# Performance work log

Measured on AMD Instinct MI355X. Metric: run time of the kernel, lower is better.

Reference implementation:

```python
import jax, jax.numpy as jnp
import numpy as np

EPS = 1e-5  # torch LayerNorm default

def _std(x):
    # standardize over the last 3 (tensor-feature) modes, biased variance like torch LayerNorm
    mu = jnp.mean(x, axis=(-3, -2, -1), keepdims=True)
    var = jnp.mean(jnp.square(x - mu), axis=(-3, -2, -1), keepdims=True)
    return (x - mu) * jax.lax.rsqrt(var + EPS)

def setup_inputs() -> dict:
    key = jax.random.key(0)
    ks = jax.random.split(key, 12)
    T, B = 512, 16
    a = b = c = 16          # input tensor modes (4096 features)
    ha = hb = hc = 8        # hidden tensor modes (512 features)
    G = 3                   # gates: r, z, n
    f32 = jnp.float32
    return {
        "x": jax.random.normal(ks[0], (T, B, a, b, c), f32),
        "h0": jnp.zeros((B, ha, hb, hc), f32),
        # input-to-hidden TCL3D factors + rank-1 bias + LN affines (stacked over 3 gates)
        "W_fa": jax.random.normal(ks[1], (G, a, ha), f32),
        "W_fb": jax.random.normal(ks[2], (G, b, hb), f32),
        "W_fc": jax.random.normal(ks[3], (G, c, hc), f32),
        "W_ba": jax.random.normal(ks[4], (G, ha), f32),
        "W_bb": jax.random.normal(ks[5], (G, hb), f32),
        "W_bc": jax.random.normal(ks[6], (G, hc), f32),
        "W_lnin_w": jnp.ones((G, a, b, c), f32),
        "W_lnin_b": jnp.zeros((G, a, b, c), f32),
        "W_lnout_w": jnp.ones((G, ha, hb, hc), f32),
        "W_lnout_b": jnp.zeros((G, ha, hb, hc), f32),
        # hidden-to-hidden TCL3D factors + rank-1 bias + LN affines
        "U_fa": jax.random.normal(ks[7], (G, ha, ha), f32),
        "U_fb": jax.random.normal(ks[8], (G, hb, hb), f32),
        "U_fc": jax.random.normal(ks[9], (G, hc, hc), f32),
        "U_ba": jax.random.normal(ks[10], (G, ha), f32),
        "U_bb": jax.random.normal(ks[11], (G, hb), f32),
        "U_bc": jax.random.normal(jax.random.fold_in(key, 99), (G, hc), f32),
        "U_lnin_w": jnp.ones((G, ha, hb, hc), f32),
        "U_lnin_b": jnp.zeros((G, ha, hb, hc), f32),
        "U_lnout_w": jnp.ones((G, ha, hb, hc), f32),
        "U_lnout_b": jnp.zeros((G, ha, hb, hc), f32),
    }

def reference(x, h0, W_fa, W_fb, W_fc, W_ba, W_bb, W_bc,
              W_lnin_w, W_lnin_b, W_lnout_w, W_lnout_b,
              U_fa, U_fb, U_fc, U_ba, U_bb, U_bc,
              U_lnin_w, U_lnin_b, U_lnout_w, U_lnout_b):
    # --- input-to-hidden TCL3D for all 3 gates, batched over time (no h dependence) ---
    xh = _std(x)                                                  # [T,B,a,b,c]
    xg = xh[None] * W_lnin_w[:, None, None] + W_lnin_b[:, None, None]  # [3,T,B,a,b,c]
    Wx = jnp.einsum('gtnabc,gad,gbe,gcf->gtndef', xg, W_fa, W_fb, W_fc)
    Wx = Wx + (W_ba[:, None, None, :, None, None]
               * W_bb[:, None, None, None, :, None]
               * W_bc[:, None, None, None, None, :])              # rank-1 bias
    Wx = _std(Wx) * W_lnout_w[:, None, None] + W_lnout_b[:, None, None]
    Wx = jnp.swapaxes(Wx, 0, 1)                                   # [T,3,B,ha,hb,hc]

    Ub = (U_ba[:, None, :, None, None]
          * U_bb[:, None, None, :, None]
          * U_bc[:, None, None, None, :])                         # [3,1,ha,hb,hc]

    def step(h, wx):
        # hidden-to-hidden TCL3D for all 3 gates
        hh = _std(h)                                              # [B,ha,hb,hc]
        hg = hh[None] * U_lnin_w[:, None] + U_lnin_b[:, None]     # [3,B,ha,hb,hc]
        Uh = jnp.einsum('gndef,gdp,geq,gfr->gnpqr', hg, U_fa, U_fb, U_fc) + Ub
        Uh = _std(Uh) * U_lnout_w[:, None] + U_lnout_b[:, None]
        r = jax.nn.sigmoid(wx[0] + Uh[0])
        z = jax.nn.sigmoid(wx[1] + Uh[1])
        n = jnp.tanh(wx[2] + r * Uh[2])
        h_new = (1.0 - z) * n + z * h
        return h_new, h_new

    _, outs = jax.lax.scan(step, h0, Wx)                          # [T,B,ha,hb,hc]
    return outs
```

## Files before the change

### kernel.cpp

```cpp
#include <hip/hip_runtime.h>

#define EPSV 1e-5f

#define KEEPV(x) asm volatile("" : "+v"(x))
#define KEEPS(x) asm volatile("" : "+s"(x))

#define DPP_XADD(v, ctrl)                                                  \
    v += __int_as_float(__builtin_amdgcn_update_dpp(                       \
        0, __float_as_int(v), ctrl, 0xF, 0xF, false))

__device__ __forceinline__ float wave_allsum(float v) {
    DPP_XADD(v, 0x128);
    DPP_XADD(v, 0x124);
    DPP_XADD(v, 0x122);
    DPP_XADD(v, 0x121);
    DPP_XADD(v, 0x142);
    DPP_XADD(v, 0x143);
    return __int_as_float(__builtin_amdgcn_readlane(__float_as_int(v), 63));
}

__device__ __forceinline__ void bar_lds() {
    asm volatile("s_waitcnt lgkmcnt(0)\n\ts_barrier" ::: "memory");
}

__global__ __launch_bounds__(256) void wx_kernel(
    const float* __restrict__ x,
    const float* __restrict__ Wfa, const float* __restrict__ Wfb,
    const float* __restrict__ Wfc,
    const float* __restrict__ Wba, const float* __restrict__ Wbb,
    const float* __restrict__ Wbc,
    const float* __restrict__ lniw, const float* __restrict__ lnib,
    const float* __restrict__ lnow, const float* __restrict__ lnob,
    float* __restrict__ wxo)
{
    __shared__ float Xs[4096];
    __shared__ float S1[2048];
    __shared__ float S2[1024];
    __shared__ float baS[24], bbS[24], bcS[24];
    __shared__ float red[16];

    const int tid  = threadIdx.x;
    const int wid  = tid >> 6, lane = tid & 63;
    const size_t tb = blockIdx.x;
    const float* xp = x + tb * 4096;

    float s = 0.f, s2 = 0.f;
    for (int i = tid; i < 4096; i += 256) {
        float v = xp[i];
        Xs[i] = v;
        s += v; s2 += v * v;
    }
    if (tid < 24) { baS[tid] = Wba[tid]; bbS[tid] = Wbb[tid]; bcS[tid] = Wbc[tid]; }

    __syncthreads();
    #pragma unroll
    for (int off = 32; off > 0; off >>= 1) {
        s  += __shfl_down(s,  off);
        s2 += __shfl_down(s2, off);
    }
    if (lane == 0) { red[wid] = s; red[8 + wid] = s2; }
    __syncthreads();
    s  = red[0] + red[1] + red[2] + red[3];
    s2 = red[8] + red[9] + red[10] + red[11];
    const float muX = s * (1.f / 4096.f);
    const float rsX = rsqrtf(fmaxf(s2 * (1.f / 4096.f) - muX * muX, 0.f) + EPSV);

    const int qh = __builtin_amdgcn_readfirstlane(tid >> 7);
    const int rh = __builtin_amdgcn_readfirstlane(tid >> 6);

    for (int g = 0; g < 3; ++g) {
        {
            float acc[8] = {0,0,0,0,0,0,0,0};
            const int rest = tid;
            const float* lw = lniw + g * 4096;
            const float* lb = lnib + g * 4096;
            #pragma unroll
            for (int m = 0; m < 16; ++m) {
                const float xn = (Xs[m*256 + rest] - muX) * rsX;
                const float xv = fmaf(xn, lw[m*256 + rest], lb[m*256 + rest]);
                #pragma unroll
                for (int p = 0; p < 8; ++p)
                    acc[p] = fmaf(xv, Wfa[(g*16 + m)*8 + p], acc[p]);
            }
            #pragma unroll
            for (int p = 0; p < 8; ++p)
                S1[p*256 + (rest ^ (p << 3))] = acc[p];
        }
        __syncthreads();
        {
            float acc[4] = {0,0,0,0};
            const int rest2 = tid & 127;
            const int c2 = rest2 >> 3, p2 = rest2 & 7;
            #pragma unroll
            for (int m = 0; m < 16; ++m) {
                const float xv = S1[p2*256 + (((m << 4) | c2) ^ (p2 << 3))];
                #pragma unroll
                for (int j = 0; j < 4; ++j)
                    acc[j] = fmaf(xv, Wfb[(g*16 + m)*8 + qh*4 + j], acc[j]);
            }
            #pragma unroll
            for (int j = 0; j < 4; ++j) {
                const int q = qh*4 + j;
                S2[q*128 + (rest2 ^ (q << 3))] = acc[j];
            }
        }
        __syncthreads();
        float v0, v1; int idx0;
        {
            float acc[2] = {0, 0};
            const int rest3 = tid & 63;
            const int q3 = rest3 & 7, pp = rest3 >> 3;
            #pragma unroll
            for (int m = 0; m < 16; ++m) {
                const float xv = S2[q3*128 + (((m << 3) | pp) ^ (q3 << 3))];
                #pragma unroll
                for (int j = 0; j < 2; ++j)
                    acc[j] = fmaf(xv, Wfc[(g*16 + m)*8 + rh*2 + j], acc[j]);
            }
            const float bpq = baS[g*8 + pp] * bbS[g*8 + q3];
            v0 = acc[0] + bpq * bcS[g*8 + rh*2 + 0];
            v1 = acc[1] + bpq * bcS[g*8 + rh*2 + 1];
            idx0 = rest3 * 8 + rh * 2;
        }
        float t = v0 + v1, t2 = v0*v0 + v1*v1;
        __syncthreads();
        #pragma unroll
        for (int off = 32; off > 0; off >>= 1) {
            t  += __shfl_down(t,  off);
            t2 += __shfl_down(t2, off);
        }
        if (lane == 0) { red[wid] = t; red[8 + wid] = t2; }
        __syncthreads();
        t  = red[0] + red[1] + red[2] + red[3];
        t2 = red[8] + red[9] + red[10] + red[11];
        const float mu  = t * (1.f / 512.f);
        const float var = fmaxf(t2 * (1.f / 512.f) - mu * mu, 0.f);
        const float rs  = rsqrtf(var + EPSV);
        float* wp = wxo + (tb * 3 + g) * 512;
        const float2 lw2 = *(const float2*)(lnow + g*512 + idx0);
        const float2 lb2 = *(const float2*)(lnob + g*512 + idx0);
        float2 o2;
        o2.x = fmaf((v0 - mu) * rs, lw2.x, lb2.x);
        o2.y = fmaf((v1 - mu) * rs, lw2.y, lb2.y);
        *(float2*)(wp + idx0) = o2;
    }
}

__global__ __launch_bounds__(192)
__attribute__((amdgpu_waves_per_eu(1, 1)))
void scan_kernel(
    const float* __restrict__ wx,
    const float* __restrict__ h0,
    const float* __restrict__ Ufa, const float* __restrict__ Ufb,
    const float* __restrict__ Ufc,
    const float* __restrict__ Uba, const float* __restrict__ Ubb,
    const float* __restrict__ Ubc,
    const float* __restrict__ lniw, const float* __restrict__ lnib,
    const float* __restrict__ lnow, const float* __restrict__ lnob,
    float* __restrict__ out,
    int T, int B)
{
    const int n    = blockIdx.x;
    const int tid  = threadIdx.x;
    const int lane = tid & 63;
    const int gu   = __builtin_amdgcn_readfirstlane(tid >> 6);

    __shared__ float hgS[3][576];
    __shared__ float T1S[3][576];
    __shared__ float T2S[3][576];
    __shared__ float UhS[2][3][576];

    float wA[64], wB[64], wC[64];
    #pragma unroll
    for (int i = 0; i < 64; ++i) {
        wA[i] = __uint_as_float(__builtin_amdgcn_readfirstlane(
                    __float_as_uint(Ufa[gu*64 + i])));
        KEEPS(wA[i]);
    }
    #pragma unroll
    for (int i = 0; i < 64; ++i) { wB[i] = Ufb[gu*64 + i]; KEEPV(wB[i]); }
    #pragma unroll
    for (int i = 0; i < 64; ++i) { wC[i] = Ufc[gu*64 + i]; KEEPV(wC[i]); }

    float lnwT[8], lnbT[8], low8[8], lob8[8], ubias[8];
    {
        const int p_ = lane >> 3, q_ = lane & 7;
        const float bpq = Uba[gu*8 + p_] * Ubb[gu*8 + q_];
        #pragma unroll
        for (int k = 0; k < 8; ++k) {
            lnwT[k]  = lniw[gu*512 + k*64 + lane];
            lnbT[k]  = lnib[gu*512 + k*64 + lane];
            low8[k]  = lnow[gu*512 + lane*8 + k];
            lob8[k]  = lnob[gu*512 + lane*8 + k];
            ubias[k] = bpq * Ubc[gu*8 + k];
        }
    }

    const int wbase = lane;
    const int rbase = (lane & 7) * 72 + (lane >> 3);

    float hv[8];
    {
        const float4 a = *(const float4*)(h0 + n*512 + lane*8);
        const float4 b = *(const float4*)(h0 + n*512 + lane*8 + 4);
        hv[0]=a.x; hv[1]=a.y; hv[2]=a.z; hv[3]=a.w;
        hv[4]=b.x; hv[5]=b.y; hv[6]=b.z; hv[7]=b.w;
    }

    float uo[8];
    float pf[3][8];

#define LOADWX(TT)                                                         \
    {                                                                      \
        const float* base_ = wx + (((size_t)(TT) * B + n) * 3) * 512       \
                             + lane * 8;                                   \
        _Pragma("unroll")                                                  \
        for (int gg = 0; gg < 3; ++gg) {                                   \
            const float4 A_ = *(const float4*)(base_ + gg*512);            \
            const float4 B_ = *(const float4*)(base_ + gg*512 + 4);        \
            pf[gg][0]=A_.x; pf[gg][1]=A_.y; pf[gg][2]=A_.z; pf[gg][3]=A_.w;\
            pf[gg][4]=B_.x; pf[gg][5]=B_.y; pf[gg][6]=B_.z; pf[gg][7]=B_.w;\
        }                                                                  \
    }

#define WR8(BUFROW, V)                                                     \
    {                                                                      \
        float* p0_ = (BUFROW) + wbase;                                     \
        float* p1_ = p0_ + 288;                                            \
        p0_[0] = V[0]; p0_[72] = V[1]; p0_[144] = V[2]; p0_[216] = V[3];   \
        p1_[0] = V[4]; p1_[72] = V[5]; p1_[144] = V[6]; p1_[216] = V[7];   \
    }

#define RD8(BUFROW, V)                                                     \
    {                                                                      \
        const float* q_ = (BUFROW) + rbase;                                \
        V[0] = q_[0];  V[1] = q_[8];  V[2] = q_[16]; V[3] = q_[24];        \
        V[4] = q_[32]; V[5] = q_[40]; V[6] = q_[48]; V[7] = q_[56];        \
    }

#define RD8W(BUFROW, V)                                                    \
    {                                                                      \
        const float* q0_ = (BUFROW) + wbase;                               \
        const float* q1_ = q0_ + 288;                                      \
        V[0] = q0_[0]; V[1] = q0_[72]; V[2] = q0_[144]; V[3] = q0_[216];   \
        V[4] = q1_[0]; V[5] = q1_[72]; V[6] = q1_[144]; V[7] = q1_[216];   \
    }

#define PIPELINE(PARN)                                                     \
    {                                                                      \
         \
         \
        float xv_[8];                                                      \
        RD8(hgS[gu], xv_)                                                  \
        float sA = 0.f, sB = 0.f;                                          \
        _Pragma("unroll")                                                  \
        for (int k = 0; k < 8; ++k) { sA += hv[k]; sB += hv[k]*hv[k]; }    \
        sA = wave_allsum(sA); sB = wave_allsum(sB);                        \
        const float mu_ = sA * (1.f/512.f);                                \
        const float rs_ = rsqrtf(fmaxf(sB*(1.f/512.f) - mu_*mu_, 0.f)      \
                                 + EPSV);                                  \
        float a_[8];                                                       \
        _Pragma("unroll") for (int k = 0; k < 8; ++k) a_[k] = 0.f;         \
        _Pragma("unroll")                                                  \
        for (int m = 0; m < 8; ++m) {                                      \
            const float hgv = fmaf((xv_[m]-mu_)*rs_, lnwT[m], lnbT[m]);    \
            _Pragma("unroll")                                              \
            for (int q = 0; q < 8; ++q)                                    \
                a_[q] = fmaf(hgv, wA[m*8 + q], a_[q]);                     \
        }                                                                  \
        WR8(T1S[gu], a_)                                                   \
        RD8(T1S[gu], xv_)                                                  \
        _Pragma("unroll") for (int k = 0; k < 8; ++k) a_[k] = 0.f;         \
        _Pragma("unroll")                                                  \
        for (int m = 0; m < 8; ++m) {                                      \
            _Pragma("unroll")                                              \
            for (int q = 0; q < 8; ++q)                                    \
                a_[q] = fmaf(xv_[m], wB[m*8 + q], a_[q]);                  \
        }                                                                  \
        WR8(T2S[gu], a_)                                                   \
        RD8(T2S[gu], xv_)                                                  \
        _Pragma("unroll") for (int k = 0; k < 8; ++k) a_[k] = 0.f;         \
        _Pragma("unroll")                                                  \
        for (int m = 0; m < 8; ++m) {                                      \
            _Pragma("unroll")                                              \
            for (int q = 0; q < 8; ++q)                                    \
                a_[q] = fmaf(xv_[m], wC[m*8 + q], a_[q]);                  \
        }                                                                  \
        float sC = 0.f, sD = 0.f;                                          \
        _Pragma("unroll")                                                  \
        for (int k = 0; k < 8; ++k) {                                      \
            a_[k] += ubias[k]; sC += a_[k]; sD += a_[k]*a_[k];             \
        }                                                                  \
        sC = wave_allsum(sC); sD = wave_allsum(sD);                        \
        const float mu2_ = sC * (1.f/512.f);                               \
        const float rs2_ = rsqrtf(fmaxf(sD*(1.f/512.f) - mu2_*mu2_, 0.f)   \
                                  + EPSV);                                 \
        _Pragma("unroll")                                                  \
        for (int k = 0; k < 8; ++k)                                        \
            uo[k] = fmaf((a_[k]-mu2_)*rs2_, low8[k], lob8[k]);             \
        WR8(UhS[PARN][gu], uo)                                             \
    }

#define COMBINE(PARC, TT)                                                  \
    {                                                                      \
        float ur[8], uz[8], un[8];                                         \
        if (gu == 0) {                                                     \
            _Pragma("unroll")                                              \
            for (int k = 0; k < 8; ++k) ur[k] = uo[k];                     \
            RD8W(UhS[PARC][1], uz)                                         \
            RD8W(UhS[PARC][2], un)                                         \
        } else if (gu == 1) {                                              \
            _Pragma("unroll")                                              \
            for (int k = 0; k < 8; ++k) uz[k] = uo[k];                     \
            RD8W(UhS[PARC][0], ur)                                         \
            RD8W(UhS[PARC][2], un)                                         \
        } else {                                                           \
            _Pragma("unroll")                                              \
            for (int k = 0; k < 8; ++k) un[k] = uo[k];                     \
            RD8W(UhS[PARC][0], ur)                                         \
            RD8W(UhS[PARC][1], uz)                                         \
        }                                                                  \
        _Pragma("unroll")                                                  \
        for (int k = 0; k < 8; ++k) {                                      \
            const float er_ = __expf(-(pf[0][k] + ur[k]));                 \
            const float r_  = __builtin_amdgcn_rcpf(1.f + er_);            \
            const float ez_ = __expf(-(pf[1][k] + uz[k]));                 \
            const float z_  = __builtin_amdgcn_rcpf(1.f + ez_);            \
            const float e2_ = __expf(2.f * (pf[2][k] + r_ * un[k]));       \
            const float nn_ = 1.f - 2.f*__builtin_amdgcn_rcpf(e2_ + 1.f);  \
            hv[k] = (1.f - z_)*nn_ + z_*hv[k];                             \
        }                                                                  \
        WR8(hgS[gu], hv)      \
        if (gu == 0) {                                                     \
            float* op_ = out + ((size_t)(TT) * B + n) * 512 + lane*8;      \
            *(float4*)op_     = make_float4(hv[0], hv[1], hv[2], hv[3]);   \
            *(float4*)(op_+4) = make_float4(hv[4], hv[5], hv[6], hv[7]);   \
        }                                                                  \
    }

    LOADWX(0);
    WR8(hgS[gu], hv)
    PIPELINE(0);

    for (int t = 0; t < T; t += 2) {
        bar_lds();
        COMBINE(0, t)
        if (t + 1 < T) {
            LOADWX(t + 1);
            PIPELINE(1)
        }
        bar_lds();
        if (t + 1 < T) COMBINE(1, t + 1)
        if (t + 2 < T) {
            LOADWX(t + 2);
            PIPELINE(0)
        }
    }
#undef LOADWX
#undef WR8
#undef RD8
#undef RD8W
#undef PIPELINE
#undef COMBINE
}

extern "C" void kernel_launch(void* const* d_in, const int* in_sizes, int n_in,
                              void* d_out, int out_size, void* d_ws, size_t ws_size,
                              hipStream_t stream)
{
    const float* x    = (const float*)d_in[0];
    const float* h0   = (const float*)d_in[1];
    const float* Wfa  = (const float*)d_in[2];
    const float* Wfb  = (const float*)d_in[3];
    const float* Wfc  = (const float*)d_in[4];
    const float* Wba  = (const float*)d_in[5];
    const float* Wbb  = (const float*)d_in[6];
    const float* Wbc  = (const float*)d_in[7];
    const float* Wliw = (const float*)d_in[8];
    const float* Wlib = (const float*)d_in[9];
    const float* Wlow = (const float*)d_in[10];
    const float* Wlob = (const float*)d_in[11];
    const float* Ufa  = (const float*)d_in[12];
    const float* Ufb  = (const float*)d_in[13];
    const float* Ufc  = (const float*)d_in[14];
    const float* Uba  = (const float*)d_in[15];
    const float* Ubb  = (const float*)d_in[16];
    const float* Ubc  = (const float*)d_in[17];
    const float* Uliw = (const float*)d_in[18];
    const float* Ulib = (const float*)d_in[19];
    const float* Ulow = (const float*)d_in[20];
    const float* Ulob = (const float*)d_in[21];

    const int B = in_sizes[1] / 512;
    const int T = in_sizes[0] / (B * 4096);

    float* wxws = (float*)d_ws;
    float* out  = (float*)d_out;

    wx_kernel<<<T * B, 256, 0, stream>>>(x, Wfa, Wfb, Wfc, Wba, Wbb, Wbc,
                                         Wliw, Wlib, Wlow, Wlob, wxws);
    scan_kernel<<<B, 192, 0, stream>>>(wxws, h0, Ufa, Ufb, Ufc, Uba, Ubb, Ubc,
                                       Uliw, Ulib, Ulow, Ulob, out, T, B);
}
```

Measured before the change: 805.7 us.

## Process all three gates together in wx_kernel and vectorize input loads

The input-projection kernel now computes all three gates in a single pass through each TCL stage instead of looping over gates. This cuts the block-wide barriers from about four per gate to three in total, and each normalized x value is read from LDS once instead of three times. The input tile is loaded with float4 loads, and the shared buffers are pooled so S2 reuses the Xs region. The trade-off is more live accumulators per thread and a larger LDS footprint, which could lower occupancy.

```diff
diff --git a/kernel.cpp b/kernel.cpp
--- a/kernel.cpp
+++ b/kernel.cpp
@@ -33,11 +33,13 @@
     const float* __restrict__ lnow, const float* __restrict__ lnob,
     float* __restrict__ wxo)
 {
-    __shared__ float Xs[4096];
-    __shared__ float S1[2048];
-    __shared__ float S2[1024];
+    __shared__ float POOL[4096 + 3*2048];
     __shared__ float baS[24], bbS[24], bcS[24];
-    __shared__ float red[16];
+    __shared__ float red[48];
+
+    float* Xs = POOL;
+    float* S1 = POOL + 4096;
+    float* S2 = POOL;
 
     const int tid  = threadIdx.x;
     const int wid  = tid >> 6, lane = tid & 63;
@@ -45,14 +47,14 @@
     const float* xp = x + tb * 4096;
 
     float s = 0.f, s2 = 0.f;
-    for (int i = tid; i < 4096; i += 256) {
-        float v = xp[i];
-        Xs[i] = v;
-        s += v; s2 += v * v;
+    for (int i = tid; i < 1024; i += 256) {
+        const float4 v4 = ((const float4*)xp)[i];
+        ((float4*)Xs)[i] = v4;
+        s  += v4.x + v4.y + v4.z + v4.w;
+        s2 += v4.x*v4.x + v4.y*v4.y + v4.z*v4.z + v4.w*v4.w;
     }
     if (tid < 24) { baS[tid] = Wba[tid]; bbS[tid] = Wbb[tid]; bcS[tid] = Wbc[tid]; }
 
-    __syncthreads();
     #pragma unroll
     for (int off = 32; off > 0; off >>= 1) {
         s  += __shfl_down(s,  off);
@@ -68,81 +70,127 @@
     const int qh = __builtin_amdgcn_readfirstlane(tid >> 7);
     const int rh = __builtin_amdgcn_readfirstlane(tid >> 6);
 
-    for (int g = 0; g < 3; ++g) {
-        {
-            float acc[8] = {0,0,0,0,0,0,0,0};
-            const int rest = tid;
-            const float* lw = lniw + g * 4096;
-            const float* lb = lnib + g * 4096;
-            #pragma unroll
-            for (int m = 0; m < 16; ++m) {
-                const float xn = (Xs[m*256 + rest] - muX) * rsX;
-                const float xv = fmaf(xn, lw[m*256 + rest], lb[m*256 + rest]);
+    {
+        float acc[3][8];
+        #pragma unroll
+        for (int g = 0; g < 3; ++g)
+            #pragma unroll
+            for (int p = 0; p < 8; ++p) acc[g][p] = 0.f;
+        const int rest = tid;
+        #pragma unroll
+        for (int m = 0; m < 16; ++m) {
+            const float xn = (Xs[m*256 + rest] - muX) * rsX;
+            #pragma unroll
+            for (int g = 0; g < 3; ++g) {
+                const float xv = fmaf(xn, lniw[g*4096 + m*256 + rest],
+                                      lnib[g*4096 + m*256 + rest]);
                 #pragma unroll
                 for (int p = 0; p < 8; ++p)
-                    acc[p] = fmaf(xv, Wfa[(g*16 + m)*8 + p], acc[p]);
-            }
+                    acc[g][p] = fmaf(xv, Wfa[(g*16 + m)*8 + p], acc[g][p]);
+            }
+        }
+        #pragma unroll
+        for (int g = 0; g < 3; ++g)
             #pragma unroll
             for (int p = 0; p < 8; ++p)
-                S1[p*256 + (rest ^ (p << 3))] = acc[p];
-        }
-        __syncthreads();
-        {
-            float acc[4] = {0,0,0,0};
-            const int rest2 = tid & 127;
-            const int c2 = rest2 >> 3, p2 = rest2 & 7;
-            #pragma unroll
-            for (int m = 0; m < 16; ++m) {
-                const float xv = S1[p2*256 + (((m << 4) | c2) ^ (p2 << 3))];
+                S1[g*2048 + p*256 + (rest ^ (p << 3))] = acc[g][p];
+    }
+    __syncthreads();
+
+    {
+        float acc[3][4];
+        #pragma unroll
+        for (int g = 0; g < 3; ++g)
+            #pragma unroll
+            for (int j = 0; j < 4; ++j) acc[g][j] = 0.f;
+        const int rest2 = tid & 127;
+        const int c2 = rest2 >> 3, p2 = rest2 & 7;
+        #pragma unroll
+        for (int m = 0; m < 16; ++m) {
+            const int off1 = p2*256 + (((m << 4) | c2) ^ (p2 << 3));
+            #pragma unroll
+            for (int g = 0; g < 3; ++g) {
+                const float xv = S1[g*2048 + off1];
                 #pragma unroll
                 for (int j = 0; j < 4; ++j)
-                    acc[j] = fmaf(xv, Wfb[(g*16 + m)*8 + qh*4 + j], acc[j]);
-            }
+                    acc[g][j] = fmaf(xv, Wfb[(g*16 + m)*8 + qh*4 + j], acc[g][j]);
+            }
+        }
+        #pragma unroll
+        for (int g = 0; g < 3; ++g)
             #pragma unroll
             for (int j = 0; j < 4; ++j) {
                 const int q = qh*4 + j;
-                S2[q*128 + (rest2 ^ (q << 3))] = acc[j];
-            }
-        }
-        __syncthreads();
-        float v0, v1; int idx0;
-        {
-            float acc[2] = {0, 0};
-            const int rest3 = tid & 63;
-            const int q3 = rest3 & 7, pp = rest3 >> 3;
-            #pragma unroll
-            for (int m = 0; m < 16; ++m) {
-                const float xv = S2[q3*128 + (((m << 3) | pp) ^ (q3 << 3))];
+                S2[g*1024 + q*128 + (rest2 ^ (q << 3))] = acc[g][j];
+            }
+    }
+    __syncthreads();
+
+    float v0[3], v1[3]; int idx0;
+    {
+        const int rest3 = tid & 63;
+        const int q3 = rest3 & 7, pp = rest3 >> 3;
+        float acc[3][2];
+        #pragma unroll
+        for (int g = 0; g < 3; ++g) { acc[g][0] = 0.f; acc[g][1] = 0.f; }
+        #pragma unroll
+        for (int m = 0; m < 16; ++m) {
+            const int off2 = q3*128 + (((m << 3) | pp) ^ (q3 << 3));
+            #pragma unroll
+            for (int g = 0; g < 3; ++g) {
+                const float xv = S2[g*1024 + off2];
                 #pragma unroll
                 for (int j = 0; j < 2; ++j)
-                    acc[j] = fmaf(xv, Wfc[(g*16 + m)*8 + rh*2 + j], acc[j]);
-            }
+                    acc[g][j] = fmaf(xv, Wfc[(g*16 + m)*8 + rh*2 + j], acc[g][j]);
+            }
+        }
+        #pragma unroll
+        for (int g = 0; g < 3; ++g) {
             const float bpq = baS[g*8 + pp] * bbS[g*8 + q3];
-            v0 = acc[0] + bpq * bcS[g*8 + rh*2 + 0];
-            v1 = acc[1] + bpq * bcS[g*8 + rh*2 + 1];
-            idx0 = rest3 * 8 + rh * 2;
-        }
-        float t = v0 + v1, t2 = v0*v0 + v1*v1;
+            v0[g] = acc[g][0] + bpq * bcS[g*8 + rh*2 + 0];
+            v1[g] = acc[g][1] + bpq * bcS[g*8 + rh*2 + 1];
+        }
+        idx0 = rest3 * 8 + rh * 2;
+    }
+
+    {
+        float t[3], t2[3];
+        #pragma unroll
+        for (int g = 0; g < 3; ++g) {
+            t[g]  = v0[g] + v1[g];
+            t2[g] = v0[g]*v0[g] + v1[g]*v1[g];
+        }
+        #pragma unroll
+        for (int off = 32; off > 0; off >>= 1)
+            #pragma unroll
+            for (int g = 0; g < 3; ++g) {
+                t[g]  += __shfl_down(t[g],  off);
+                t2[g] += __shfl_down(t2[g], off);
+            }
+        if (lane == 0)
+            #pragma unroll
+            for (int g = 0; g < 3; ++g) {
+                red[(g*2 + 0)*8 + wid] = t[g];
+                red[(g*2 + 1)*8 + wid] = t2[g];
+            }
         __syncthreads();
         #pragma unroll
-        for (int off = 32; off > 0; off >>= 1) {
-            t  += __shfl_down(t,  off);
-            t2 += __shfl_down(t2, off);
-        }
-        if (lane == 0) { red[wid] = t; red[8 + wid] = t2; }
-        __syncthreads();
-        t  = red[0] + red[1] + red[2] + red[3];
-        t2 = red[8] + red[9] + red[10] + red[11];
-        const float mu  = t * (1.f / 512.f);
-        const float var = fmaxf(t2 * (1.f / 512.f) - mu * mu, 0.f);
-        const float rs  = rsqrtf(var + EPSV);
-        float* wp = wxo + (tb * 3 + g) * 512;
-        const float2 lw2 = *(const float2*)(lnow + g*512 + idx0);
-        const float2 lb2 = *(const float2*)(lnob + g*512 + idx0);
-        float2 o2;
-        o2.x = fmaf((v0 - mu) * rs, lw2.x, lb2.x);
-        o2.y = fmaf((v1 - mu) * rs, lw2.y, lb2.y);
-        *(float2*)(wp + idx0) = o2;
+        for (int g = 0; g < 3; ++g) {
+            const float ts  = red[(g*2+0)*8+0] + red[(g*2+0)*8+1]
+                            + red[(g*2+0)*8+2] + red[(g*2+0)*8+3];
+            const float t2s = red[(g*2+1)*8+0] + red[(g*2+1)*8+1]
+                            + red[(g*2+1)*8+2] + red[(g*2+1)*8+3];
+            const float mu  = ts * (1.f / 512.f);
+            const float var = fmaxf(t2s * (1.f / 512.f) - mu * mu, 0.f);
+            const float rs  = rsqrtf(var + EPSV);
+            float* wp = wxo + (tb * 3 + g) * 512;
+            const float2 lw2 = *(const float2*)(lnow + g*512 + idx0);
+            const float2 lb2 = *(const float2*)(lnob + g*512 + idx0);
+            float2 o2;
+            o2.x = fmaf((v0[g] - mu) * rs, lw2.x, lb2.x);
+            o2.y = fmaf((v1[g] - mu) * rs, lw2.y, lb2.y);
+            *(float2*)(wp + idx0) = o2;
+        }
     }
 }
 
@@ -248,8 +296,6 @@
 
 #define PIPELINE(PARN)                                                     \
     {                                                                      \
-         \
-         \
         float xv_[8];                                                      \
         RD8(hgS[gu], xv_)                                                  \
         float sA = 0.f, sB = 0.f;                                          \
```

After: 797.7 us, median of 2. About the same (-1.0%).
